# Performance work log

Hardware: AMD Instinct MI355X
Metric: run time of the kernel (lower is better)

The kernel has to match this reference:

```python
import jax, jax.numpy as jnp
import numpy as np

NUM_SLOTS = 8
SLOT_DIM = 64
HIDDEN_DIM = 128  # max(slot_dim, 128)
ITERS = 3
EPS = 1e-08
LN_EPS = 1e-05


def _ln(x, w, b):
    mu = jnp.mean(x, axis=-1, keepdims=True)
    var = jnp.mean(jnp.square(x - mu), axis=-1, keepdims=True)
    return (x - mu) * jax.lax.rsqrt(var + LN_EPS) * w + b


def setup_inputs() -> dict:
    key = jax.random.key(0)
    ks = jax.random.split(key, 16)
    b, n, d, h, n_s = 64, 4096, SLOT_DIM, HIDDEN_DIM, NUM_SLOTS
    s = 1.0 / np.sqrt(d)
    sh = 1.0 / np.sqrt(h)
    inp = {
        'inputs': jax.random.normal(ks[0], (b, n, d), jnp.float32),
        'mask': jax.random.randint(ks[1], (b, n), 0, 2, jnp.int32),
        'noise': jax.random.normal(ks[2], (b, n_s, d), jnp.float32),
        'slots_mu': jax.random.normal(ks[3], (1, 1, d), jnp.float32),
        'slots_sigma': jax.random.uniform(ks[4], (1, 1, d), jnp.float32),
        'Wq': jax.random.normal(ks[5], (d, d), jnp.float32) * s,
        'bq': jnp.zeros((d,), jnp.float32),
        'Wk': jax.random.normal(ks[6], (d, d), jnp.float32) * s,
        'bk': jnp.zeros((d,), jnp.float32),
        'Wv': jax.random.normal(ks[7], (d, d), jnp.float32) * s,
        'bv': jnp.zeros((d,), jnp.float32),
        'W_ih': jax.random.normal(ks[8], (3 * d, d), jnp.float32) * s,
        'b_ih': jnp.zeros((3 * d,), jnp.float32),
        'W_hh': jax.random.normal(ks[9], (3 * d, d), jnp.float32) * s,
        'b_hh': jnp.zeros((3 * d,), jnp.float32),
        'W1': jax.random.normal(ks[10], (h, d), jnp.float32) * s,
        'b1': jnp.zeros((h,), jnp.float32),
        'W2': jax.random.normal(ks[11], (d, h), jnp.float32) * sh,
        'b2': jnp.zeros((d,), jnp.float32),
        'ln_in_w': jnp.ones((d,), jnp.float32), 'ln_in_b': jnp.zeros((d,), jnp.float32),
        'ln_s_w': jnp.ones((d,), jnp.float32), 'ln_s_b': jnp.zeros((d,), jnp.float32),
        'ln_ff_w': jnp.ones((d,), jnp.float32), 'ln_ff_b': jnp.zeros((d,), jnp.float32),
    }
    return inp


def reference(inputs, mask, noise, slots_mu, slots_sigma, Wq, bq, Wk, bk, Wv, bv,
              W_ih, b_ih, W_hh, b_hh, W1, b1, W2, b2,
              ln_in_w, ln_in_b, ln_s_w, ln_s_b, ln_ff_w, ln_ff_b):
    b, n, d = inputs.shape
    scale = d ** (-0.5)
    # slots ~ Normal(mu, sigma) via reparameterization with fixed noise
    slots = slots_mu + slots_sigma * noise  # [b, n_s, d]
    m = (mask[:, :, None] != 0)  # [b, n, 1]
    x = _ln(inputs, ln_in_w, ln_in_b)
    k = x @ Wk.T + bk  # [b, n, d]
    v = x @ Wv.T + bv  # [b, n, d]
    for _ in range(ITERS):
        slots_prev = slots
        s_n = _ln(slots, ln_s_w, ln_s_b)
        q = s_n @ Wq.T + bq  # [b, n_s, d]
        dots = jnp.einsum('bid,bjd->bij', k, q) * scale  # [b, n, n_s]
        attn = jax.nn.softmax(dots, axis=-1) + EPS
        attn = jnp.where(m, attn, 0.0)
        attn = attn / jnp.sum(attn, axis=-2, keepdims=True)
        updates = jnp.einsum('bij,bid->bjd', attn, v)  # [b, n_s, d]
        # GRUCell(updates, slots_prev)
        gx = updates @ W_ih.T + b_ih  # [b, n_s, 3d]
        gh = slots_prev @ W_hh.T + b_hh
        xr, xz, xn = jnp.split(gx, 3, axis=-1)
        hr, hz, hn = jnp.split(gh, 3, axis=-1)
        r = jax.nn.sigmoid(xr + hr)
        z = jax.nn.sigmoid(xz + hz)
        nn_ = jnp.tanh(xn + r * hn)
        slots = (1.0 - z) * nn_ + z * slots_prev
        # residual MLP
        ff = _ln(slots, ln_ff_w, ln_ff_b)
        slots = slots + (jax.nn.relu(ff @ W1.T + b1) @ W2.T + b2)
    return slots
```

## Files before the change

### kernel.cpp

```cpp
#include <hip/hip_runtime.h>
#include <hip/hip_bf16.h>

typedef unsigned short u16;
typedef unsigned int u32;

#define BB 64
#define NN 4096
#define DD 64
#define NSLOT 8
#define HH 128
#define NITER 3

#define BF16_ONES_PROBE 0x3F803F80u

#define OFF_WQ   0
#define OFF_WK   4096
#define OFF_WV   8192
#define OFF_WIH  12288
#define OFF_WHH  24576
#define OFF_W1   36864
#define OFF_W2   45056
#define OFF_BQ   53248
#define OFF_BK   53312
#define OFF_BV   53376
#define OFF_BIH  53440
#define OFF_BHH  53632
#define OFF_B1   53824
#define OFF_B2   53952
#define OFF_LIW  54016
#define OFF_LIB  54080
#define OFF_LSW  54144
#define OFF_LSB  54208
#define OFF_LFW  54272
#define OFF_LFB  54336
#define OFF_WKT  54400
#define OFF_PK   58496

__device__ __forceinline__ float bf2f(u16 u) {
    union { u32 i; float f; } c; c.i = ((u32)u) << 16; return c.f;
}
__device__ __forceinline__ float bflo(u32 u) {
    union { u32 i; float f; } c; c.i = u << 16; return c.f;
}
__device__ __forceinline__ float bfhi(u32 u) {
    union { u32 i; float f; } c; c.i = u & 0xffff0000u; return c.f;
}
__device__ __forceinline__ u16 f2bf(float f) {
    __hip_bfloat16 h = __float2bfloat16(f);
    return *reinterpret_cast<u16*>(&h);
}
__device__ __forceinline__ float ldf(const void* p, int i, bool isbf) {
    return isbf ? bf2f(((const u16*)p)[i]) : ((const float*)p)[i];
}

__device__ __forceinline__ float wsum64(float x) {
    #pragma unroll
    for (int o = 32; o > 0; o >>= 1) x += __shfl_xor(x, o);
    return x;
}

__device__ __forceinline__ float ln64(float v, const float* __restrict__ g,
                                      const float* __restrict__ b, int lane) {
    float mu = wsum64(v) * (1.f / 64.f);
    float d = v - mu;
    float var = wsum64(d * d) * (1.f / 64.f);
    return d * rsqrtf(var + 1e-5f) * g[lane] + b[lane];
}

__device__ __forceinline__ float mat64p(float xv, const float* __restrict__ P, int lane) {
    const float4* p4 = (const float4*)P;
    float acc = 0.f;
    #pragma unroll
    for (int c = 0; c < 16; c++) {
        float4 w = p4[c * 64 + lane];
        acc += w.x * __shfl(xv, 4 * c + 0) + w.y * __shfl(xv, 4 * c + 1)
             + w.z * __shfl(xv, 4 * c + 2) + w.w * __shfl(xv, 4 * c + 3);
    }
    return acc;
}

struct ConvArgs {
    const void* src[20];
    int off[20];
    int n[20];
};

__global__ __launch_bounds__(256) void conv_w(ConvArgs a, float* __restrict__ wf,
                                              const u32* __restrict__ probe) {
    bool isbf = (*probe == BF16_ONES_PROBE);
    int t = blockIdx.y;
    int idx = blockIdx.x * 256 + threadIdx.x;
    if (idx < a.n[t]) wf[a.off[t] + idx] = ldf(a.src[t], idx, isbf);
}

__global__ __launch_bounds__(256) void transp_wk(float* __restrict__ wf) {
    int idx = blockIdx.x * 256 + threadIdx.x;
    int i = idx >> 6, j = idx & 63;
    wf[OFF_WKT + i * 64 + j] = wf[OFF_WK + j * 64 + i];
}

__global__ __launch_bounds__(256) void repack_w(float* __restrict__ wf) {
    const int srcs[13] = {OFF_WV, OFF_WQ, OFF_WKT,
                          OFF_WIH, OFF_WIH + 4096, OFF_WIH + 8192,
                          OFF_WHH, OFF_WHH + 4096, OFF_WHH + 8192,
                          OFF_W1, OFF_W1 + 4096,
                          OFF_W2, OFF_W2 + 64};
    const int strd[13] = {64, 64, 64, 64, 64, 64, 64, 64, 64, 64, 64, 128, 128};
    int idx = blockIdx.x * 256 + threadIdx.x;
    if (idx >= 13 * 4096) return;
    int blk = idx >> 12, r = idx & 4095;
    int c = r >> 8, rem = r & 255, j = rem >> 2, d = rem & 3;
    wf[OFF_PK + idx] = wf[srcs[blk] + j * strd[blk] + 4 * c + d];
}

__global__ __launch_bounds__(64) void init_slots(
        const void* __restrict__ noise, const void* __restrict__ mu, const void* __restrict__ sg,
        const float* __restrict__ wf, float* __restrict__ slots,
        float* __restrict__ qk, float* __restrict__ bkdot,
        float* __restrict__ upd, float* __restrict__ sums, const u32* __restrict__ probe) {
    bool isbf = (*probe == BF16_ONES_PROBE);
    int bs = blockIdx.x;
    int i = threadIdx.x;
    int idx = bs * DD + i;
    float sl = ldf(mu, i, isbf) + ldf(sg, i, isbf) * ldf(noise, idx, isbf);
    slots[idx] = sl;
    upd[idx] = 0.f;
    if (i == 0) sums[bs] = 0.f;
    float sn = ln64(sl, wf + OFF_LSW, wf + OFF_LSB, i);
    float qv = wf[OFF_BQ + i] + mat64p(sn, wf + OFF_PK + 1 * 4096, i);
    qk[idx] = mat64p(qv, wf + OFF_PK + 2 * 4096, i);
    float bd = wsum64(qv * wf[OFF_BK + i]);
    if (i == 0) bkdot[bs] = bd;
}

__global__ __launch_bounds__(256) void ln_x(
        const void* __restrict__ xin, const float* __restrict__ wf,
        u16* __restrict__ xnb, const u32* __restrict__ probe) {
    bool isbf = (*probe == BF16_ONES_PROBE);
    int lane = threadIdx.x & 63;
    size_t tok = ((size_t)blockIdx.x << 2) + (threadIdx.x >> 6);
    size_t off = tok * 64 + lane;
    float x = isbf ? bf2f(((const u16*)xin)[off]) : ((const float*)xin)[off];
    float muv = wsum64(x) * (1.f / 64.f);
    float d = x - muv;
    float var = wsum64(d * d) * (1.f / 64.f);
    float xn = d * rsqrtf(var + 1e-5f) * wf[OFF_LIW + lane] + wf[OFF_LIB + lane];
    xnb[off] = f2bf(xn);
}

__global__ __launch_bounds__(256) void attn_pass1(
        const u16* __restrict__ xnb, const float* __restrict__ qk,
        const float* __restrict__ bkdot, const int* __restrict__ mask,
        float* __restrict__ attn) {
    int b = blockIdx.x >> 4;
    int tok = ((blockIdx.x & 15) << 8) + threadIdx.x;
    size_t g = ((size_t)b << 12) + tok;
    const float* qkb = qk + (b << 9);
    const float* bkb = bkdot + (b << 3);
    float d[8];
    #pragma unroll
    for (int s = 0; s < 8; s++) d[s] = bkb[s];
    const uint4* kr = (const uint4*)(xnb + g * 64);
    #pragma unroll
    for (int c = 0; c < 8; c++) {
        uint4 u = kr[c];
        float kf[8];
        kf[0] = bflo(u.x); kf[1] = bfhi(u.x); kf[2] = bflo(u.y); kf[3] = bfhi(u.y);
        kf[4] = bflo(u.z); kf[5] = bfhi(u.z); kf[6] = bflo(u.w); kf[7] = bfhi(u.w);
        #pragma unroll
        for (int s = 0; s < 8; s++) {
            const float* qs = qkb + s * 64 + c * 8;
            #pragma unroll
            for (int uu = 0; uu < 8; uu++) d[s] += kf[uu] * qs[uu];
        }
    }
    #pragma unroll
    for (int s = 0; s < 8; s++) d[s] *= 0.125f;

    float mx = d[0];
    #pragma unroll
    for (int s = 1; s < 8; s++) mx = fmaxf(mx, d[s]);
    float den = 0.f;
    #pragma unroll
    for (int s = 0; s < 8; s++) { d[s] = expf(d[s] - mx); den += d[s]; }
    float inv = 1.f / den;
    int mk = mask[g];
    #pragma unroll
    for (int s = 0; s < 8; s++) d[s] = (mk != 0) ? (d[s] * inv + 1e-8f) : 0.f;

    float4* ar = (float4*)(attn + g * 8);
    float4 s0; s0.x = d[0]; s0.y = d[1]; s0.z = d[2]; s0.w = d[3];
    float4 s1; s1.x = d[4]; s1.y = d[5]; s1.z = d[6]; s1.w = d[7];
    ar[0] = s0; ar[1] = s1;
}

__global__ __launch_bounds__(256) void attn_pass2(
        const u16* __restrict__ xnb, const float* __restrict__ attn,
        float* __restrict__ upd, float* __restrict__ sums) {
    __shared__ float red[4][NSLOT][64];
    __shared__ float red2[4][NSLOT];
    int b = blockIdx.x >> 4;
    int wave = threadIdx.x >> 6;
    int lane = threadIdx.x & 63;
    size_t base = ((size_t)b << 12) + ((blockIdx.x & 15) << 8) + (wave << 6);
    float acc[8] = {0.f, 0.f, 0.f, 0.f, 0.f, 0.f, 0.f, 0.f};
    float ss[8]  = {0.f, 0.f, 0.f, 0.f, 0.f, 0.f, 0.f, 0.f};
    #pragma unroll 8
    for (int t = 0; t < 64; t++) {
        size_t g = base + t;
        float vv = bf2f(xnb[g * 64 + lane]);
        const float* ar = attn + g * 8;
        #pragma unroll
        for (int s = 0; s < 8; s++) { float a = ar[s]; acc[s] += a * vv; ss[s] += a; }
    }
    #pragma unroll
    for (int s = 0; s < 8; s++) red[wave][s][lane] = acc[s];
    if (lane == 0) {
        #pragma unroll
        for (int s = 0; s < 8; s++) red2[wave][s] = ss[s];
    }
    __syncthreads();
    if (wave == 0) {
        float* ur = upd + (size_t)b * NSLOT * DD;
        #pragma unroll
        for (int s = 0; s < 8; s++) {
            float v = red[0][s][lane] + red[1][s][lane] + red[2][s][lane] + red[3][s][lane];
            atomicAdd(ur + s * 64 + lane, v);
        }
        if (lane < NSLOT) {
            float t = red2[0][lane] + red2[1][lane] + red2[2][lane] + red2[3][lane];
            atomicAdd(sums + b * NSLOT + lane, t);
        }
    }
}

__global__ __launch_bounds__(64) void finalize_k(
        const float* __restrict__ wf, float* __restrict__ upd, float* __restrict__ sums,
        float* __restrict__ slots, float* __restrict__ qk, float* __restrict__ bkdot,
        void* __restrict__ out, int last, const u32* __restrict__ probe) {
    bool isbf = (*probe == BF16_ONES_PROBE);
    int bs = blockIdx.x;
    int i = threadIdx.x;
    int idx = bs * DD + i;
    const float* P = wf + OFF_PK;

    float sm = sums[bs];
    float un = upd[idx] / sm;
    upd[idx] = 0.f;
    if (i == 0) sums[bs] = 0.f;

    float uv = wf[OFF_BV + i] + mat64p(un, P + 0 * 4096, i);

    float sp = slots[idx];

    float gxr = wf[OFF_BIH + i], gxz = wf[OFF_BIH + 64 + i], gxn = wf[OFF_BIH + 128 + i];
    float ghr = wf[OFF_BHH + i], ghz = wf[OFF_BHH + 64 + i], ghn = wf[OFF_BHH + 128 + i];
    const float4* pxr = (const float4*)(P + 3 * 4096);
    const float4* pxz = (const float4*)(P + 4 * 4096);
    const float4* pxn = (const float4*)(P + 5 * 4096);
    const float4* phr = (const float4*)(P + 6 * 4096);
    const float4* phz = (const float4*)(P + 7 * 4096);
    const float4* phn = (const float4*)(P + 8 * 4096);
    #pragma unroll
    for (int c = 0; c < 16; c++) {
        float u0 = __shfl(uv, 4 * c + 0), u1 = __shfl(uv, 4 * c + 1);
        float u2 = __shfl(uv, 4 * c + 2), u3 = __shfl(uv, 4 * c + 3);
        float p0 = __shfl(sp, 4 * c + 0), p1 = __shfl(sp, 4 * c + 1);
        float p2 = __shfl(sp, 4 * c + 2), p3 = __shfl(sp, 4 * c + 3);
        float4 a;
        a = pxr[c * 64 + i]; gxr += a.x * u0 + a.y * u1 + a.z * u2 + a.w * u3;
        a = pxz[c * 64 + i]; gxz += a.x * u0 + a.y * u1 + a.z * u2 + a.w * u3;
        a = pxn[c * 64 + i]; gxn += a.x * u0 + a.y * u1 + a.z * u2 + a.w * u3;
        a = phr[c * 64 + i]; ghr += a.x * p0 + a.y * p1 + a.z * p2 + a.w * p3;
        a = phz[c * 64 + i]; ghz += a.x * p0 + a.y * p1 + a.z * p2 + a.w * p3;
        a = phn[c * 64 + i]; ghn += a.x * p0 + a.y * p1 + a.z * p2 + a.w * p3;
    }
    float r = 1.f / (1.f + expf(-(gxr + ghr)));
    float z = 1.f / (1.f + expf(-(gxz + ghz)));
    float nn = tanhf(gxn + r * ghn);
    float snew = (1.f - z) * nn + z * sp;

    float ff = ln64(snew, wf + OFF_LFW, wf + OFF_LFB, i);
    float h1a = wf[OFF_B1 + i], h1b = wf[OFF_B1 + 64 + i];
    const float4* p1a = (const float4*)(P + 9 * 4096);
    const float4* p1b = (const float4*)(P + 10 * 4096);
    #pragma unroll
    for (int c = 0; c < 16; c++) {
        float f0 = __shfl(ff, 4 * c + 0), f1 = __shfl(ff, 4 * c + 1);
        float f2 = __shfl(ff, 4 * c + 2), f3 = __shfl(ff, 4 * c + 3);
        float4 a;
        a = p1a[c * 64 + i]; h1a += a.x * f0 + a.y * f1 + a.z * f2 + a.w * f3;
        a = p1b[c * 64 + i]; h1b += a.x * f0 + a.y * f1 + a.z * f2 + a.w * f3;
    }
    h1a = fmaxf(h1a, 0.f);
    h1b = fmaxf(h1b, 0.f);
    float o = snew + wf[OFF_B2 + i];
    const float4* p2a = (const float4*)(P + 11 * 4096);
    const float4* p2b = (const float4*)(P + 12 * 4096);
    #pragma unroll
    for (int c = 0; c < 16; c++) {
        float a0 = __shfl(h1a, 4 * c + 0), a1 = __shfl(h1a, 4 * c + 1);
        float a2 = __shfl(h1a, 4 * c + 2), a3 = __shfl(h1a, 4 * c + 3);
        float b0 = __shfl(h1b, 4 * c + 0), b1 = __shfl(h1b, 4 * c + 1);
        float b2 = __shfl(h1b, 4 * c + 2), b3 = __shfl(h1b, 4 * c + 3);
        float4 a;
        a = p2a[c * 64 + i]; o += a.x * a0 + a.y * a1 + a.z * a2 + a.w * a3;
        a = p2b[c * 64 + i]; o += a.x * b0 + a.y * b1 + a.z * b2 + a.w * b3;
    }

    slots[idx] = o;
    if (last) {
        if (isbf) ((u16*)out)[idx] = f2bf(o);
        else      ((float*)out)[idx] = o;
    } else {
        float sn2 = ln64(o, wf + OFF_LSW, wf + OFF_LSB, i);
        float qv = wf[OFF_BQ + i] + mat64p(sn2, P + 1 * 4096, i);
        qk[idx] = mat64p(qv, P + 2 * 4096, i);
        float bd = wsum64(qv * wf[OFF_BK + i]);
        if (i == 0) bkdot[bs] = bd;
    }
}

extern "C" void kernel_launch(void* const* d_in, const int* in_sizes, int n_in,
                              void* d_out, int out_size, void* d_ws, size_t ws_size,
                              hipStream_t stream) {
    const void* xin  = d_in[0];
    const int* mask  = (const int*)d_in[1];
    const void* noise = d_in[2];
    const void* mu    = d_in[3];
    const void* sg    = d_in[4];
    const u32* probe  = (const u32*)d_in[19];

    char* ws = (char*)d_ws;
    float* wf = (float*)ws;

    size_t o = 524288;
    u16* xnb     = (u16*)(ws + o);   o += (size_t)BB * NN * DD * 2;
    float* attn  = (float*)(ws + o); o += (size_t)BB * NN * NSLOT * 4;
    float* qk    = (float*)(ws + o); o += (size_t)BB * NSLOT * DD * 4;
    float* bkdot = (float*)(ws + o); o += (size_t)BB * NSLOT * 4;
    float* slots = (float*)(ws + o); o += (size_t)BB * NSLOT * DD * 4;
    float* upd   = (float*)(ws + o); o += (size_t)BB * NSLOT * DD * 4;
    float* sums  = (float*)(ws + o); o += (size_t)BB * NSLOT * 4;

    static const int widx[20] = {5, 7, 9, 11, 13, 15, 17, 6, 8, 10, 12, 14, 16, 18,
                                 19, 20, 21, 22, 23, 24};
    static const int woff[20] = {OFF_WQ, OFF_WK, OFF_WV, OFF_WIH, OFF_WHH, OFF_W1, OFF_W2,
                                 OFF_BQ, OFF_BK, OFF_BV, OFF_BIH, OFF_BHH, OFF_B1, OFF_B2,
                                 OFF_LIW, OFF_LIB, OFF_LSW, OFF_LSB, OFF_LFW, OFF_LFB};
    ConvArgs ca;
    for (int j = 0; j < 20; j++) {
        ca.src[j] = d_in[widx[j]];
        ca.off[j] = woff[j];
        ca.n[j]   = in_sizes[widx[j]];
    }
    conv_w<<<dim3(48, 20), 256, 0, stream>>>(ca, wf, probe);
    transp_wk<<<16, 256, 0, stream>>>(wf);
    repack_w<<<208, 256, 0, stream>>>(wf);
    init_slots<<<BB * NSLOT, 64, 0, stream>>>(noise, mu, sg, wf, slots, qk, bkdot,
                                              upd, sums, probe);

    ln_x<<<BB * NN / 4, 256, 0, stream>>>(xin, wf, xnb, probe);

    for (int it = 0; it < NITER; it++) {
        attn_pass1<<<BB * 16, 256, 0, stream>>>(xnb, qk, bkdot, mask, attn);
        attn_pass2<<<BB * 16, 256, 0, stream>>>(xnb, attn, upd, sums);
        finalize_k<<<BB * NSLOT, 64, 0, stream>>>(wf, upd, sums, slots, qk, bkdot,
                                                  d_out, it == NITER - 1 ? 1 : 0, probe);
    }
}
```

Before: 302.0 us.

## Fold input LayerNorm into attention algebraically and fuse both attention passes

Removes the separate LayerNorm pass and the bf16 normalized-input buffer. LN is folded into the q·k dot product through precomputed gamma-scaled query vectors and per-slot constants, and into the update sum through a rank-one mean correction. The two attention passes are merged into one kernel that keeps attention weights in LDS instead of writing them to global memory. Masked tokens skip their loads. The cost is re-reading raw fp32 input each iteration instead of a half-size bf16 copy, plus a one-pass variance formula that is less numerically stable.

```diff
diff --git a/kernel.cpp b/kernel.cpp
--- a/kernel.cpp
+++ b/kernel.cpp
@@ -3,6 +3,7 @@
 
 typedef unsigned short u16;
 typedef unsigned int u32;
+typedef unsigned long long u64;
 
 #define BB 64
 #define NN 4096
@@ -39,12 +40,6 @@
 __device__ __forceinline__ float bf2f(u16 u) {
     union { u32 i; float f; } c; c.i = ((u32)u) << 16; return c.f;
 }
-__device__ __forceinline__ float bflo(u32 u) {
-    union { u32 i; float f; } c; c.i = u << 16; return c.f;
-}
-__device__ __forceinline__ float bfhi(u32 u) {
-    union { u32 i; float f; } c; c.i = u & 0xffff0000u; return c.f;
-}
 __device__ __forceinline__ u16 f2bf(float f) {
     __hip_bfloat16 h = __float2bfloat16(f);
     return *reinterpret_cast<u16*>(&h);
@@ -113,141 +108,183 @@
     wf[OFF_PK + idx] = wf[srcs[blk] + j * strd[blk] + 4 * c + d];
 }
 
+__device__ __forceinline__ void emit_qstate(
+        float qv, int b, int s, int bs, int lane, const float* __restrict__ wf,
+        float* __restrict__ gqp, float* __restrict__ Avec, float* __restrict__ Cvec) {
+    float qkv = mat64p(qv, wf + OFF_PK + 2 * 4096, lane);
+    float g_in = wf[OFF_LIW + lane];
+    float b_in = wf[OFF_LIB + lane];
+    float gqv = g_in * qkv;
+    gqp[(b << 9) + (lane >> 2) * 32 + s * 4 + (lane & 3)] = gqv;
+    float A  = wsum64(gqv);
+    float bd = wsum64(qv * wf[OFF_BK + lane]);
+    float cq = wsum64(b_in * qkv);
+    if (lane == 0) { Avec[bs] = A; Cvec[bs] = cq + bd; }
+}
+
 __global__ __launch_bounds__(64) void init_slots(
         const void* __restrict__ noise, const void* __restrict__ mu, const void* __restrict__ sg,
         const float* __restrict__ wf, float* __restrict__ slots,
-        float* __restrict__ qk, float* __restrict__ bkdot,
-        float* __restrict__ upd, float* __restrict__ sums, const u32* __restrict__ probe) {
+        float* __restrict__ gqp, float* __restrict__ Avec, float* __restrict__ Cvec,
+        float* __restrict__ acc1, float* __restrict__ ssv, float* __restrict__ A2v,
+        const u32* __restrict__ probe) {
     bool isbf = (*probe == BF16_ONES_PROBE);
     int bs = blockIdx.x;
+    int b = bs >> 3, s = bs & 7;
     int i = threadIdx.x;
     int idx = bs * DD + i;
     float sl = ldf(mu, i, isbf) + ldf(sg, i, isbf) * ldf(noise, idx, isbf);
     slots[idx] = sl;
-    upd[idx] = 0.f;
-    if (i == 0) sums[bs] = 0.f;
+    acc1[idx] = 0.f;
+    if (i == 0) { ssv[bs] = 0.f; A2v[bs] = 0.f; }
     float sn = ln64(sl, wf + OFF_LSW, wf + OFF_LSB, i);
     float qv = wf[OFF_BQ + i] + mat64p(sn, wf + OFF_PK + 1 * 4096, i);
-    qk[idx] = mat64p(qv, wf + OFF_PK + 2 * 4096, i);
-    float bd = wsum64(qv * wf[OFF_BK + i]);
-    if (i == 0) bkdot[bs] = bd;
-}
-
-__global__ __launch_bounds__(256) void ln_x(
-        const void* __restrict__ xin, const float* __restrict__ wf,
-        u16* __restrict__ xnb, const u32* __restrict__ probe) {
+    emit_qstate(qv, b, s, bs, i, wf, gqp, Avec, Cvec);
+}
+
+__global__ __launch_bounds__(256) void fused_attn(
+        const void* __restrict__ xin, const int* __restrict__ mask,
+        const float* __restrict__ gqp, const float* __restrict__ Avec,
+        const float* __restrict__ Cvec,
+        float* __restrict__ acc1, float* __restrict__ ssv, float* __restrict__ A2v,
+        const u32* __restrict__ probe) {
+    __shared__ float aw_lds[256][12];
+    __shared__ float racc[4][NSLOT][64];
+    __shared__ float rss[4][NSLOT];
+    __shared__ float rA2[4][NSLOT];
+    __shared__ u64 wmask[4];
+
     bool isbf = (*probe == BF16_ONES_PROBE);
-    int lane = threadIdx.x & 63;
-    size_t tok = ((size_t)blockIdx.x << 2) + (threadIdx.x >> 6);
-    size_t off = tok * 64 + lane;
-    float x = isbf ? bf2f(((const u16*)xin)[off]) : ((const float*)xin)[off];
-    float muv = wsum64(x) * (1.f / 64.f);
-    float d = x - muv;
-    float var = wsum64(d * d) * (1.f / 64.f);
-    float xn = d * rsqrtf(var + 1e-5f) * wf[OFF_LIW + lane] + wf[OFF_LIB + lane];
-    xnb[off] = f2bf(xn);
-}
-
-__global__ __launch_bounds__(256) void attn_pass1(
-        const u16* __restrict__ xnb, const float* __restrict__ qk,
-        const float* __restrict__ bkdot, const int* __restrict__ mask,
-        float* __restrict__ attn) {
     int b = blockIdx.x >> 4;
-    int tok = ((blockIdx.x & 15) << 8) + threadIdx.x;
-    size_t g = ((size_t)b << 12) + tok;
-    const float* qkb = qk + (b << 9);
-    const float* bkb = bkdot + (b << 3);
-    float d[8];
-    #pragma unroll
-    for (int s = 0; s < 8; s++) d[s] = bkb[s];
-    const uint4* kr = (const uint4*)(xnb + g * 64);
-    #pragma unroll
-    for (int c = 0; c < 8; c++) {
-        uint4 u = kr[c];
-        float kf[8];
-        kf[0] = bflo(u.x); kf[1] = bfhi(u.x); kf[2] = bflo(u.y); kf[3] = bfhi(u.y);
-        kf[4] = bflo(u.z); kf[5] = bfhi(u.z); kf[6] = bflo(u.w); kf[7] = bfhi(u.w);
+    int base = (blockIdx.x & 15) << 8;
+    int tid = threadIdx.x;
+    int wave = tid >> 6, lane = tid & 63;
+
+    size_t gt = ((size_t)b << 12) + base + tid;
+    int mk = mask[gt];
+    float sum = 0.f, sq = 0.f;
+    float d[8] = {0.f, 0.f, 0.f, 0.f, 0.f, 0.f, 0.f, 0.f};
+    const float4* gq4 = (const float4*)(gqp + ((size_t)b << 9));
+    if (mk) {
+        if (isbf) {
+            const ushort4* xr = (const ushort4*)((const u16*)xin + gt * 64);
+            #pragma unroll
+            for (int c = 0; c < 16; c++) {
+                ushort4 u = xr[c];
+                float x0 = bf2f(u.x), x1 = bf2f(u.y), x2 = bf2f(u.z), x3 = bf2f(u.w);
+                sum += x0 + x1 + x2 + x3;
+                sq += x0 * x0 + x1 * x1 + x2 * x2 + x3 * x3;
+                #pragma unroll
+                for (int s = 0; s < 8; s++) {
+                    float4 q = gq4[c * 8 + s];
+                    d[s] += q.x * x0 + q.y * x1 + q.z * x2 + q.w * x3;
+                }
+            }
+        } else {
+            const float4* xr = (const float4*)((const float*)xin + gt * 64);
+            #pragma unroll
+            for (int c = 0; c < 16; c++) {
+                float4 xv = xr[c];
+                sum += xv.x + xv.y + xv.z + xv.w;
+                sq += xv.x * xv.x + xv.y * xv.y + xv.z * xv.z + xv.w * xv.w;
+                #pragma unroll
+                for (int s = 0; s < 8; s++) {
+                    float4 q = gq4[c * 8 + s];
+                    d[s] += q.x * xv.x + q.y * xv.y + q.z * xv.z + q.w * xv.w;
+                }
+            }
+        }
+    }
+    float muv = sum * (1.f / 64.f);
+    float var = sq * (1.f / 64.f) - muv * muv;
+    float rs = rsqrtf(var + 1e-5f);
+    const float* Av = Avec + (b << 3);
+    const float* Cv = Cvec + (b << 3);
+    #pragma unroll
+    for (int s = 0; s < 8; s++)
+        d[s] = 0.125f * (rs * d[s] - rs * muv * Av[s] + Cv[s]);
+
+    float mx = d[0];
+    #pragma unroll
+    for (int s = 1; s < 8; s++) mx = fmaxf(mx, d[s]);
+    float den = 0.f;
+    #pragma unroll
+    for (int s = 0; s < 8; s++) { d[s] = expf(d[s] - mx); den += d[s]; }
+    float inv = 1.f / den;
+    float attn[8], aw[8];
+    #pragma unroll
+    for (int s = 0; s < 8; s++) {
+        attn[s] = (mk != 0) ? (d[s] * inv + 1e-8f) : 0.f;
+        aw[s] = attn[s] * rs;
+    }
+    {
+        float4 w0; w0.x = aw[0]; w0.y = aw[1]; w0.z = aw[2]; w0.w = aw[3];
+        float4 w1; w1.x = aw[4]; w1.y = aw[5]; w1.z = aw[6]; w1.w = aw[7];
+        *(float4*)&aw_lds[tid][0] = w0;
+        *(float4*)&aw_lds[tid][4] = w1;
+    }
+    u64 bal = __ballot(mk != 0);
+    if (lane == 0) wmask[wave] = bal;
+    #pragma unroll
+    for (int s = 0; s < 8; s++) {
+        float t1 = wsum64(attn[s]);
+        float t2 = wsum64(aw[s] * muv);
+        if (lane == 0) { rss[wave][s] = t1; rA2[wave][s] = t2; }
+    }
+    __syncthreads();
+
+    u64 bits = wmask[wave];
+    float acc[8] = {0.f, 0.f, 0.f, 0.f, 0.f, 0.f, 0.f, 0.f};
+    size_t rowbase = ((size_t)b << 12) + base + (wave << 6);
+    #pragma unroll 4
+    for (int t = 0; t < 64; t++) {
+        if ((bits >> t) & 1ULL) {
+            float xv = isbf ? bf2f(((const u16*)xin)[(rowbase + t) * 64 + lane])
+                            : ((const float*)xin)[(rowbase + t) * 64 + lane];
+            const float4* ap = (const float4*)&aw_lds[(wave << 6) + t][0];
+            float4 a0 = ap[0], a1 = ap[1];
+            acc[0] += a0.x * xv; acc[1] += a0.y * xv; acc[2] += a0.z * xv; acc[3] += a0.w * xv;
+            acc[4] += a1.x * xv; acc[5] += a1.y * xv; acc[6] += a1.z * xv; acc[7] += a1.w * xv;
+        }
+    }
+    #pragma unroll
+    for (int s = 0; s < 8; s++) racc[wave][s][lane] = acc[s];
+    __syncthreads();
+    if (wave == 0) {
+        float* ag = acc1 + ((size_t)b << 9);
         #pragma unroll
         for (int s = 0; s < 8; s++) {
-            const float* qs = qkb + s * 64 + c * 8;
-            #pragma unroll
-            for (int uu = 0; uu < 8; uu++) d[s] += kf[uu] * qs[uu];
-        }
-    }
-    #pragma unroll
-    for (int s = 0; s < 8; s++) d[s] *= 0.125f;
-
-    float mx = d[0];
-    #pragma unroll
-    for (int s = 1; s < 8; s++) mx = fmaxf(mx, d[s]);
-    float den = 0.f;
-    #pragma unroll
-    for (int s = 0; s < 8; s++) { d[s] = expf(d[s] - mx); den += d[s]; }
-    float inv = 1.f / den;
-    int mk = mask[g];
-    #pragma unroll
-    for (int s = 0; s < 8; s++) d[s] = (mk != 0) ? (d[s] * inv + 1e-8f) : 0.f;
-
-    float4* ar = (float4*)(attn + g * 8);
-    float4 s0; s0.x = d[0]; s0.y = d[1]; s0.z = d[2]; s0.w = d[3];
-    float4 s1; s1.x = d[4]; s1.y = d[5]; s1.z = d[6]; s1.w = d[7];
-    ar[0] = s0; ar[1] = s1;
-}
-
-__global__ __launch_bounds__(256) void attn_pass2(
-        const u16* __restrict__ xnb, const float* __restrict__ attn,
-        float* __restrict__ upd, float* __restrict__ sums) {
-    __shared__ float red[4][NSLOT][64];
-    __shared__ float red2[4][NSLOT];
-    int b = blockIdx.x >> 4;
-    int wave = threadIdx.x >> 6;
-    int lane = threadIdx.x & 63;
-    size_t base = ((size_t)b << 12) + ((blockIdx.x & 15) << 8) + (wave << 6);
-    float acc[8] = {0.f, 0.f, 0.f, 0.f, 0.f, 0.f, 0.f, 0.f};
-    float ss[8]  = {0.f, 0.f, 0.f, 0.f, 0.f, 0.f, 0.f, 0.f};
-    #pragma unroll 8
-    for (int t = 0; t < 64; t++) {
-        size_t g = base + t;
-        float vv = bf2f(xnb[g * 64 + lane]);
-        const float* ar = attn + g * 8;
-        #pragma unroll
-        for (int s = 0; s < 8; s++) { float a = ar[s]; acc[s] += a * vv; ss[s] += a; }
-    }
-    #pragma unroll
-    for (int s = 0; s < 8; s++) red[wave][s][lane] = acc[s];
-    if (lane == 0) {
-        #pragma unroll
-        for (int s = 0; s < 8; s++) red2[wave][s] = ss[s];
-    }
-    __syncthreads();
-    if (wave == 0) {
-        float* ur = upd + (size_t)b * NSLOT * DD;
-        #pragma unroll
-        for (int s = 0; s < 8; s++) {
-            float v = red[0][s][lane] + red[1][s][lane] + red[2][s][lane] + red[3][s][lane];
-            atomicAdd(ur + s * 64 + lane, v);
+            float v = racc[0][s][lane] + racc[1][s][lane] + racc[2][s][lane] + racc[3][s][lane];
+            atomicAdd(ag + s * 64 + lane, v);
         }
         if (lane < NSLOT) {
-            float t = red2[0][lane] + red2[1][lane] + red2[2][lane] + red2[3][lane];
-            atomicAdd(sums + b * NSLOT + lane, t);
+            float t1 = rss[0][lane] + rss[1][lane] + rss[2][lane] + rss[3][lane];
+            float t2 = rA2[0][lane] + rA2[1][lane] + rA2[2][lane] + rA2[3][lane];
+            atomicAdd(ssv + (b << 3) + lane, t1);
+            atomicAdd(A2v + (b << 3) + lane, t2);
         }
     }
 }
 
 __global__ __launch_bounds__(64) void finalize_k(
-        const float* __restrict__ wf, float* __restrict__ upd, float* __restrict__ sums,
-        float* __restrict__ slots, float* __restrict__ qk, float* __restrict__ bkdot,
+        const float* __restrict__ wf, float* __restrict__ acc1, float* __restrict__ ssv,
+        float* __restrict__ A2v, float* __restrict__ slots,
+        float* __restrict__ gqp, float* __restrict__ Avec, float* __restrict__ Cvec,
         void* __restrict__ out, int last, const u32* __restrict__ probe) {
     bool isbf = (*probe == BF16_ONES_PROBE);
     int bs = blockIdx.x;
+    int b = bs >> 3, s = bs & 7;
     int i = threadIdx.x;
     int idx = bs * DD + i;
     const float* P = wf + OFF_PK;
 
-    float sm = sums[bs];
-    float un = upd[idx] / sm;
-    upd[idx] = 0.f;
-    if (i == 0) sums[bs] = 0.f;
+    float sm = ssv[bs];
+    float a2 = A2v[bs];
+    float ac = acc1[idx];
+    acc1[idx] = 0.f;
+    if (i == 0) { ssv[bs] = 0.f; A2v[bs] = 0.f; }
+
+    float un = wf[OFF_LIW + i] * (ac - a2) / sm + wf[OFF_LIB + i];
 
     float uv = wf[OFF_BV + i] + mat64p(un, P + 0 * 4096, i);
 
@@ -300,11 +337,11 @@
     #pragma unroll
     for (int c = 0; c < 16; c++) {
         float a0 = __shfl(h1a, 4 * c + 0), a1 = __shfl(h1a, 4 * c + 1);
-        float a2 = __shfl(h1a, 4 * c + 2), a3 = __shfl(h1a, 4 * c + 3);
+        float a2_ = __shfl(h1a, 4 * c + 2), a3 = __shfl(h1a, 4 * c + 3);
         float b0 = __shfl(h1b, 4 * c + 0), b1 = __shfl(h1b, 4 * c + 1);
         float b2 = __shfl(h1b, 4 * c + 2), b3 = __shfl(h1b, 4 * c + 3);
         float4 a;
-        a = p2a[c * 64 + i]; o += a.x * a0 + a.y * a1 + a.z * a2 + a.w * a3;
+        a = p2a[c * 64 + i]; o += a.x * a0 + a.y * a1 + a.z * a2_ + a.w * a3;
         a = p2b[c * 64 + i]; o += a.x * b0 + a.y * b1 + a.z * b2 + a.w * b3;
     }
 
@@ -315,9 +352,7 @@
     } else {
         float sn2 = ln64(o, wf + OFF_LSW, wf + OFF_LSB, i);
         float qv = wf[OFF_BQ + i] + mat64p(sn2, P + 1 * 4096, i);
-        qk[idx] = mat64p(qv, P + 2 * 4096, i);
-        float bd = wsum64(qv * wf[OFF_BK + i]);
-        if (i == 0) bkdot[bs] = bd;
+        emit_qstate(qv, b, s, bs, i, wf, gqp, Avec, Cvec);
     }
 }
 
@@ -335,13 +370,13 @@
     float* wf = (float*)ws;
 
     size_t o = 524288;
-    u16* xnb     = (u16*)(ws + o);   o += (size_t)BB * NN * DD * 2;
-    float* attn  = (float*)(ws + o); o += (size_t)BB * NN * NSLOT * 4;
-    float* qk    = (float*)(ws + o); o += (size_t)BB * NSLOT * DD * 4;
-    float* bkdot = (float*)(ws + o); o += (size_t)BB * NSLOT * 4;
+    float* gqp   = (float*)(ws + o); o += (size_t)BB * 512 * 4;
+    float* Avec  = (float*)(ws + o); o += (size_t)BB * NSLOT * 4;
+    float* Cvec  = (float*)(ws + o); o += (size_t)BB * NSLOT * 4;
+    float* acc1  = (float*)(ws + o); o += (size_t)BB * NSLOT * DD * 4;
+    float* ssv   = (float*)(ws + o); o += (size_t)BB * NSLOT * 4;
+    float* A2v   = (float*)(ws + o); o += (size_t)BB * NSLOT * 4;
     float* slots = (float*)(ws + o); o += (size_t)BB * NSLOT * DD * 4;
-    float* upd   = (float*)(ws + o); o += (size_t)BB * NSLOT * DD * 4;
-    float* sums  = (float*)(ws + o); o += (size_t)BB * NSLOT * 4;
 
     static const int widx[20] = {5, 7, 9, 11, 13, 15, 17, 6, 8, 10, 12, 14, 16, 18,
                                  19, 20, 21, 22, 23, 24};
@@ -357,15 +392,14 @@
     conv_w<<<dim3(48, 20), 256, 0, stream>>>(ca, wf, probe);
     transp_wk<<<16, 256, 0, stream>>>(wf);
     repack_w<<<208, 256, 0, stream>>>(wf);
-    init_slots<<<BB * NSLOT, 64, 0, stream>>>(noise, mu, sg, wf, slots, qk, bkdot,
-                                              upd, sums, probe);
-
-    ln_x<<<BB * NN / 4, 256, 0, stream>>>(xin, wf, xnb, probe);
+    init_slots<<<BB * NSLOT, 64, 0, stream>>>(noise, mu, sg, wf, slots,
+                                              gqp, Avec, Cvec, acc1, ssv, A2v, probe);
 
     for (int it = 0; it < NITER; it++) {
-        attn_pass1<<<BB * 16, 256, 0, stream>>>(xnb, qk, bkdot, mask, attn);
-        attn_pass2<<<BB * 16, 256, 0, stream>>>(xnb, attn, upd, sums);
-        finalize_k<<<BB * NSLOT, 64, 0, stream>>>(wf, upd, sums, slots, qk, bkdot,
+        fused_attn<<<BB * 16, 256, 0, stream>>>(xin, mask, gqp, Avec, Cvec,
+                                                acc1, ssv, A2v, probe);
+        finalize_k<<<BB * NSLOT, 64, 0, stream>>>(wf, acc1, ssv, A2v, slots,
+                                                  gqp, Avec, Cvec,
                                                   d_out, it == NITER - 1 ? 1 : 0, probe);
     }
 }
```

Result: faster. 279.8 us (-7.4%).
